# Kernel optimization log

Hardware: AMD Instinct MI355X
Metric: run time of the kernel (lower is better)

Reference implementation:

```python
import jax, jax.numpy as jnp
import numpy as np

N_NODES = 50000


def setup_inputs() -> dict:
    key = jax.random.key(0)
    k1, k2, k3, k4, k5, k6 = jax.random.split(key, 6)
    N, E, D, F = 50000, 800000, 512, 256
    feature_ori = jax.random.normal(k1, (N, D), dtype=jnp.float32)
    feature_aug = jax.random.normal(k2, (N, D), dtype=jnp.float32)
    edge_row = jax.random.randint(k3, (E,), 0, N, dtype=jnp.int32)
    edge_col = jax.random.randint(k4, (E,), 0, N, dtype=jnp.int32)
    edge_val = jax.random.uniform(k5, (E,), dtype=jnp.float32)
    # kaiming-uniform-ish init for weight, zeros for bias (as in reset_parameters)
    bound = float(np.sqrt(6.0 / D))
    weight = jax.random.uniform(k6, (D, F), dtype=jnp.float32, minval=-bound, maxval=bound)
    bias = jnp.zeros((F,), dtype=jnp.float32)
    return {
        "feature_ori": feature_ori,
        "feature_aug": feature_aug,
        "edge_row": edge_row,
        "edge_col": edge_col,
        "edge_val": edge_val,
        "weight": weight,
        "bias": bias,
    }


def _branch(feat, weight, bias, edge_row, edge_col, edge_val):
    # support = X @ W  -> [N, F]
    support = feat @ weight
    # sparse aggregation: out[i] = sum_{e: row[e]=i} val[e] * support[col[e]]
    msgs = edge_val[:, None] * support[edge_col]          # [E, F]
    out = jax.ops.segment_sum(msgs, edge_row, num_segments=N_NODES)
    return jax.nn.relu(out + bias)


def reference(feature_ori, feature_aug, edge_row, edge_col, edge_val, weight, bias):
    out_ori = _branch(feature_ori, weight, bias, edge_row, edge_col, edge_val)
    out_aug = _branch(feature_aug, weight, bias, edge_row, edge_col, edge_val)
    return (out_ori, out_aug)
```

## Files before the change

kernel.cpp:

```cpp
#include <hip/hip_runtime.h>
#include <hip/hip_bf16.h>

#define NNODES 50000
#define NEDGES 800000
#define DIN    512
#define FOUT   256

typedef __attribute__((ext_vector_type(8))) short short8;
typedef __attribute__((ext_vector_type(4))) float f32x4;
typedef __attribute__((ext_vector_type(4))) unsigned int u32x4;
typedef __attribute__((ext_vector_type(4))) unsigned short usv4;
typedef __attribute__((ext_vector_type(8))) unsigned short usv8;

static __device__ __forceinline__ unsigned short f2bf(float f) {
    unsigned int u = __float_as_uint(f);
    u += 0x7FFF + ((u >> 16) & 1);
    return (unsigned short)(u >> 16);
}
static __device__ __forceinline__ float bf2f(unsigned short h) {
    return __uint_as_float(((unsigned int)h) << 16);
}

__global__ void prep_kernel(const float* __restrict__ W, unsigned short* __restrict__ Wt,
                            const int* __restrict__ row, int* __restrict__ cnt) {
    int b = blockIdx.x;
    if (b < 512) {
        int o = b * 256 + threadIdx.x;
        int n = o >> 9, k = o & 511;
        Wt[o] = f2bf(W[k * FOUT + n]);
    } else {
        int e = (b - 512) * 256 + threadIdx.x;
        if (e < NEDGES) atomicAdd(&cnt[row[e]], 1);
    }
}

__global__ void scan_partial(const int* __restrict__ cnt, int* __restrict__ partial) {
    __shared__ int sm[256];
    int i = blockIdx.x * 256 + threadIdx.x;
    int v = (i < NNODES) ? cnt[i] : 0;
    sm[threadIdx.x] = v; __syncthreads();
    for (int s = 128; s > 0; s >>= 1) {
        if (threadIdx.x < s) sm[threadIdx.x] += sm[threadIdx.x + s];
        __syncthreads();
    }
    if (threadIdx.x == 0) partial[blockIdx.x] = sm[0];
}

__global__ void scan_exclusive_small(int* __restrict__ partial, int nb) {
    __shared__ int sm[256];
    int t = threadIdx.x;
    int v = (t < nb) ? partial[t] : 0;
    sm[t] = v; __syncthreads();
    for (int off = 1; off < 256; off <<= 1) {
        int add = (t >= off) ? sm[t - off] : 0;
        __syncthreads();
        sm[t] += add;
        __syncthreads();
    }
    if (t < nb) partial[t] = sm[t] - v;
}

__global__ void scan_write(const int* __restrict__ cnt, const int* __restrict__ partial,
                           int* __restrict__ row_start, int* __restrict__ cursor) {
    __shared__ int sm[256];
    int t = threadIdx.x;
    int i = blockIdx.x * 256 + t;
    int v = (i < NNODES) ? cnt[i] : 0;
    sm[t] = v; __syncthreads();
    for (int off = 1; off < 256; off <<= 1) {
        int add = (t >= off) ? sm[t - off] : 0;
        __syncthreads();
        sm[t] += add;
        __syncthreads();
    }
    if (i < NNODES) {
        int rs = partial[blockIdx.x] + sm[t] - v;
        row_start[i] = rs;
        cursor[i] = rs;
    }
    if (i == 0) row_start[NNODES] = NEDGES;
}

__global__ void scatter_kernel(const int* __restrict__ row, const int* __restrict__ col,
                               const float* __restrict__ val,
                               int* __restrict__ cursor, unsigned int* __restrict__ cv) {
    int e = blockIdx.x * 256 + threadIdx.x;
    if (e < NEDGES) {
        int r = row[e];
        int pos = atomicAdd(&cursor[r], 1);
        unsigned int vb = f2bf(val[e]);
        cv[pos] = (vb << 16) | (unsigned int)col[e];
    }
}

__global__ __launch_bounds__(256, 3)
void gemm_kernel(const float* __restrict__ Xo, const float* __restrict__ Xa,
                 const unsigned short* __restrict__ Wt,
                 unsigned short* __restrict__ S) {
    __shared__ __align__(16) unsigned short As[2][64][40];
    __shared__ __align__(16) unsigned short Bs[2][256][40];
    const int tid = threadIdx.x;
    const int branch = blockIdx.z;
    const float* __restrict__ X = branch ? Xa : Xo;
    const int boff = branch * 256;
    const int m_base = blockIdx.x * 64;
    const int lane = tid & 63, wave = tid >> 6;
    const int wn = wave * 64;
    const int quad = lane >> 4, r16 = lane & 15;

    f32x4 acc[4][4] = {};

    const int arow = tid >> 2;
    const int acol = (tid & 3) * 8;

    const int gm = m_base + arow;
    const bool va = gm < NNODES;
    const float* pA = &X[(long)gm * DIN + acol];
    const unsigned short* pB0 = &Wt[(long)(arow) * DIN + acol];
    const unsigned short* pB1 = &Wt[(long)(64 + arow) * DIN + acol];
    const unsigned short* pB2 = &Wt[(long)(128 + arow) * DIN + acol];
    const unsigned short* pB3 = &Wt[(long)(192 + arow) * DIN + acol];

    f32x4 fa0, fa1;
    u32x4 ub0, ub1, ub2, ub3;

#define GEMM_LOAD(K0)                                                          \
    do {                                                                       \
        fa0 = va ? __builtin_nontemporal_load((const f32x4*)(pA + (K0)))       \
                 : (f32x4)0.f;                                                 \
        fa1 = va ? __builtin_nontemporal_load((const f32x4*)(pA + (K0) + 4))   \
                 : (f32x4)0.f;                                                 \
        ub0 = *(const u32x4*)(pB0 + (K0));                                     \
        ub1 = *(const u32x4*)(pB1 + (K0));                                     \
        ub2 = *(const u32x4*)(pB2 + (K0));                                     \
        ub3 = *(const u32x4*)(pB3 + (K0));                                     \
    } while (0)

#define GEMM_WRITE(B)                                                          \
    do {                                                                       \
        usv8 h;                                                                \
        h[0] = f2bf(fa0[0]); h[1] = f2bf(fa0[1]);                              \
        h[2] = f2bf(fa0[2]); h[3] = f2bf(fa0[3]);                              \
        h[4] = f2bf(fa1[0]); h[5] = f2bf(fa1[1]);                              \
        h[6] = f2bf(fa1[2]); h[7] = f2bf(fa1[3]);                              \
        *(usv8*)&As[B][arow][acol] = h;                                        \
        *(u32x4*)&Bs[B][arow][acol] = ub0;                                     \
        *(u32x4*)&Bs[B][64 + arow][acol] = ub1;                                \
        *(u32x4*)&Bs[B][128 + arow][acol] = ub2;                               \
        *(u32x4*)&Bs[B][192 + arow][acol] = ub3;                               \
    } while (0)

#define GEMM_COMPUTE(B)                                                        \
    do {                                                                       \
        short8 a_frag[4], b_frag[4];                                           \
        _Pragma("unroll")                                                      \
        for (int mi = 0; mi < 4; mi++)                                         \
            a_frag[mi] = *(const short8*)&As[B][mi * 16 + r16][quad * 8];      \
        _Pragma("unroll")                                                      \
        for (int ni = 0; ni < 4; ni++)                                         \
            b_frag[ni] = *(const short8*)&Bs[B][wn + ni * 16 + r16][quad * 8]; \
        _Pragma("unroll")                                                      \
        for (int mi = 0; mi < 4; mi++)                                         \
            _Pragma("unroll")                                                  \
            for (int ni = 0; ni < 4; ni++)                                     \
                acc[mi][ni] = __builtin_amdgcn_mfma_f32_16x16x32_bf16(         \
                    a_frag[mi], b_frag[ni], acc[mi][ni], 0, 0, 0);             \
    } while (0)

#define GEMM_BARRIER()                                                         \
    do {                                                                       \
        asm volatile("s_waitcnt lgkmcnt(0)" ::: "memory");                     \
        __builtin_amdgcn_s_barrier();                                          \
        __builtin_amdgcn_sched_barrier(0);                                     \
    } while (0)

    GEMM_LOAD(0);
    GEMM_WRITE(0);
    GEMM_LOAD(32);
    GEMM_BARRIER();

    #pragma unroll
    for (int t = 0; t < 16; ++t) {
        if (t < 15) GEMM_WRITE((t + 1) & 1);
        if (t + 2 < 16) GEMM_LOAD((t + 2) * 32);
        GEMM_COMPUTE(t & 1);
        if (t < 15) GEMM_BARRIER();
    }

#undef GEMM_LOAD
#undef GEMM_WRITE
#undef GEMM_COMPUTE
#undef GEMM_BARRIER

    #pragma unroll
    for (int mi = 0; mi < 4; mi++) {
        #pragma unroll
        for (int rr = 0; rr < 4; rr++) {
            int m = m_base + mi * 16 + quad * 4 + rr;
            if (m < NNODES) {
                #pragma unroll
                for (int ni = 0; ni < 4; ni++) {
                    int n = wn + ni * 16 + r16;
                    S[(long)m * 512 + boff + n] = f2bf(acc[mi][ni][rr]);
                }
            }
        }
    }
}

__global__ __launch_bounds__(256)
void aggregate_pass(const int* __restrict__ row_start,
                    const unsigned int* __restrict__ cv,
                    const unsigned short* __restrict__ S,
                    const float* __restrict__ bias, float* __restrict__ out,
                    const int half) {
    const int node = __builtin_amdgcn_readfirstlane(blockIdx.x * 4 + (threadIdx.x >> 6));
    if (node >= NNODES) return;
    const int lane = threadIdx.x & 63;
    const int fl = (lane & 31) * 8;
    const unsigned int sub = lane >> 5;
    const long soff = (long)half * 256 + fl;
    const int s = row_start[node], e = row_start[node + 1];

    float a0 = 0.f, a1 = 0.f, a2 = 0.f, a3 = 0.f;
    float a4 = 0.f, a5 = 0.f, a6 = 0.f, a7 = 0.f;

#define PLOAD(CW0, CW1, Q)                                                     \
    do {                                                                       \
        unsigned int cw_ = sub ? (CW1) : (CW0);                                \
        Q = *(const usv8*)&S[(long)(cw_ & 0xFFFFu) * 512 + soff];              \
    } while (0)

#define PFMA(CW0, CW1, Q)                                                      \
    do {                                                                       \
        unsigned int cw_ = sub ? (CW1) : (CW0);                                \
        float v = bf2f((unsigned short)(cw_ >> 16));                           \
        a0 = fmaf(v, bf2f((Q)[0]), a0); a1 = fmaf(v, bf2f((Q)[1]), a1);        \
        a2 = fmaf(v, bf2f((Q)[2]), a2); a3 = fmaf(v, bf2f((Q)[3]), a3);        \
        a4 = fmaf(v, bf2f((Q)[4]), a4); a5 = fmaf(v, bf2f((Q)[5]), a5);        \
        a6 = fmaf(v, bf2f((Q)[6]), a6); a7 = fmaf(v, bf2f((Q)[7]), a7);        \
    } while (0)

#define LOADG(C0, C1, C2, C3, C4, C5, C6, C7, Q0, Q1, Q2, Q3, I)               \
    do {                                                                       \
        C0 = cv[(I)];     C1 = cv[(I) + 1]; C2 = cv[(I) + 2]; C3 = cv[(I) + 3];\
        C4 = cv[(I) + 4]; C5 = cv[(I) + 5]; C6 = cv[(I) + 6]; C7 = cv[(I) + 7];\
        PLOAD(C0, C1, Q0); PLOAD(C2, C3, Q1);                                  \
        PLOAD(C4, C5, Q2); PLOAD(C6, C7, Q3);                                  \
    } while (0)

#define FMAG(C0, C1, C2, C3, C4, C5, C6, C7, Q0, Q1, Q2, Q3)                   \
    do {                                                                       \
        PFMA(C0, C1, Q0); PFMA(C2, C3, Q1);                                    \
        PFMA(C4, C5, Q2); PFMA(C6, C7, Q3);                                    \
    } while (0)

    unsigned int c0, c1, c2, c3, c4, c5, c6, c7;
    unsigned int d0, d1, d2, d3, d4, d5, d6, d7;
    usv8 qa0, qa1, qa2, qa3, qb0, qb1, qb2, qb3;

    int idx = s;
    int r = (e - s) >> 3;
    if (r > 0) {
        LOADG(c0, c1, c2, c3, c4, c5, c6, c7, qa0, qa1, qa2, qa3, idx); idx += 8; r--;
        while (r >= 2) {
            LOADG(d0, d1, d2, d3, d4, d5, d6, d7, qb0, qb1, qb2, qb3, idx); idx += 8;
            FMAG(c0, c1, c2, c3, c4, c5, c6, c7, qa0, qa1, qa2, qa3);
            LOADG(c0, c1, c2, c3, c4, c5, c6, c7, qa0, qa1, qa2, qa3, idx); idx += 8;
            FMAG(d0, d1, d2, d3, d4, d5, d6, d7, qb0, qb1, qb2, qb3);
            r -= 2;
        }
        if (r == 1) {
            LOADG(d0, d1, d2, d3, d4, d5, d6, d7, qb0, qb1, qb2, qb3, idx); idx += 8;
            FMAG(c0, c1, c2, c3, c4, c5, c6, c7, qa0, qa1, qa2, qa3);
            FMAG(d0, d1, d2, d3, d4, d5, d6, d7, qb0, qb1, qb2, qb3);
        } else {
            FMAG(c0, c1, c2, c3, c4, c5, c6, c7, qa0, qa1, qa2, qa3);
        }
    }
    for (; idx + 2 <= e; idx += 2) {
        unsigned int w0 = cv[idx], w1 = cv[idx + 1];
        usv8 q;
        PLOAD(w0, w1, q);
        PFMA(w0, w1, q);
    }
    if (idx < e) {
        unsigned int w = cv[idx];
        usv8 q = *(const usv8*)&S[(long)(w & 0xFFFFu) * 512 + soff];
        float v = sub ? 0.f : bf2f((unsigned short)(w >> 16));
        a0 = fmaf(v, bf2f(q[0]), a0); a1 = fmaf(v, bf2f(q[1]), a1);
        a2 = fmaf(v, bf2f(q[2]), a2); a3 = fmaf(v, bf2f(q[3]), a3);
        a4 = fmaf(v, bf2f(q[4]), a4); a5 = fmaf(v, bf2f(q[5]), a5);
        a6 = fmaf(v, bf2f(q[6]), a6); a7 = fmaf(v, bf2f(q[7]), a7);
    }

#undef PLOAD
#undef PFMA
#undef LOADG
#undef FMAG

    a0 += __shfl_xor(a0, 32); a1 += __shfl_xor(a1, 32);
    a2 += __shfl_xor(a2, 32); a3 += __shfl_xor(a3, 32);
    a4 += __shfl_xor(a4, 32); a5 += __shfl_xor(a5, 32);
    a6 += __shfl_xor(a6, 32); a7 += __shfl_xor(a7, 32);

    if (lane < 32) {
        f32x4 b0 = *(const f32x4*)&bias[fl];
        f32x4 b1 = *(const f32x4*)&bias[fl + 4];
        long o = (long)half * NNODES * FOUT + (long)node * FOUT + fl;
        f32x4 r0, r1;
        r0[0] = fmaxf(a0 + b0[0], 0.f); r0[1] = fmaxf(a1 + b0[1], 0.f);
        r0[2] = fmaxf(a2 + b0[2], 0.f); r0[3] = fmaxf(a3 + b0[3], 0.f);
        r1[0] = fmaxf(a4 + b1[0], 0.f); r1[1] = fmaxf(a5 + b1[1], 0.f);
        r1[2] = fmaxf(a6 + b1[2], 0.f); r1[3] = fmaxf(a7 + b1[3], 0.f);
        __builtin_nontemporal_store(r0, (f32x4*)&out[o]);
        __builtin_nontemporal_store(r1, (f32x4*)&out[o + 4]);
    }
}

extern "C" void kernel_launch(void* const* d_in, const int* in_sizes, int n_in,
                              void* d_out, int out_size, void* d_ws, size_t ws_size,
                              hipStream_t stream) {
    const float* Xo   = (const float*)d_in[0];
    const float* Xa   = (const float*)d_in[1];
    const int*   erow = (const int*)d_in[2];
    const int*   ecol = (const int*)d_in[3];
    const float* eval_= (const float*)d_in[4];
    const float* W    = (const float*)d_in[5];
    const float* bias = (const float*)d_in[6];
    float* out = (float*)d_out;

    char* ws = (char*)d_ws;
    unsigned short* S         = (unsigned short*)(ws);
    unsigned short* Wt        = (unsigned short*)(ws + 51200000);
    int*            cnt       = (int*)(ws + 51462144);
    int*            row_start = (int*)(ws + 51662144);
    int*            partial   = (int*)(ws + 51862208);
    unsigned int*   cv        = (unsigned int*)(ws + 51863232);

    (void)in_sizes; (void)n_in; (void)out_size; (void)ws_size;

    hipMemsetAsync(cnt, 0, 200000, stream);
    prep_kernel<<<3637, 256, 0, stream>>>(W, Wt, erow, cnt);
    scan_partial<<<196, 256, 0, stream>>>(cnt, partial);
    scan_exclusive_small<<<1, 256, 0, stream>>>(partial, 196);
    scan_write<<<196, 256, 0, stream>>>(cnt, partial, row_start, cnt);
    scatter_kernel<<<3125, 256, 0, stream>>>(erow, ecol, eval_, cnt, cv);

    dim3 gg(782, 1, 2);
    gemm_kernel<<<gg, 256, 0, stream>>>(Xo, Xa, Wt, S);

    aggregate_pass<<<12500, 256, 0, stream>>>(row_start, cv, S, bias, out, 0);
    aggregate_pass<<<12500, 256, 0, stream>>>(row_start, cv, S, bias, out, 1);
}
```

Measured before the change: 484.8 us.

## Enlarge GEMM block tile to 128x256 with 2x2 wave layout

The GEMM block tile grows from 64 rows to 128 rows. Waves are rearranged into a 2x2 grid, each computing 64x128 with 32 accumulators. This halves the number of blocks and the redundant W-tile loads per output row, and raises MFMA work per LDS fragment load. In exchange it uses more registers and LDS per block, lowers occupancy (launch bounds 3 to 2), and leaves fewer blocks for tail balancing.

```diff
diff --git a/kernel.cpp b/kernel.cpp
--- a/kernel.cpp
+++ b/kernel.cpp
@@ -93,35 +93,31 @@
     }
 }
 
-__global__ __launch_bounds__(256, 3)
+__global__ __launch_bounds__(256, 2)
 void gemm_kernel(const float* __restrict__ Xo, const float* __restrict__ Xa,
                  const unsigned short* __restrict__ Wt,
                  unsigned short* __restrict__ S) {
-    __shared__ __align__(16) unsigned short As[2][64][40];
+    __shared__ __align__(16) unsigned short As[2][128][40];
     __shared__ __align__(16) unsigned short Bs[2][256][40];
     const int tid = threadIdx.x;
     const int branch = blockIdx.z;
     const float* __restrict__ X = branch ? Xa : Xo;
     const int boff = branch * 256;
-    const int m_base = blockIdx.x * 64;
+    const int m_base = blockIdx.x * 128;
     const int lane = tid & 63, wave = tid >> 6;
-    const int wn = wave * 64;
+    const int wm = (wave >> 1) * 64, wn = (wave & 1) * 128;
     const int quad = lane >> 4, r16 = lane & 15;
 
-    f32x4 acc[4][4] = {};
-
-    const int arow = tid >> 2;
-    const int acol = (tid & 3) * 8;
-
+    f32x4 acc[4][8] = {};
+
+    const int arow = tid >> 1;
+    const int acol = (tid & 1) * 16;
     const int gm = m_base + arow;
     const bool va = gm < NNODES;
     const float* pA = &X[(long)gm * DIN + acol];
-    const unsigned short* pB0 = &Wt[(long)(arow) * DIN + acol];
-    const unsigned short* pB1 = &Wt[(long)(64 + arow) * DIN + acol];
-    const unsigned short* pB2 = &Wt[(long)(128 + arow) * DIN + acol];
-    const unsigned short* pB3 = &Wt[(long)(192 + arow) * DIN + acol];
-
-    f32x4 fa0, fa1;
+    const unsigned short* pB = &Wt[(long)tid * DIN];
+
+    f32x4 fa0, fa1, fa2, fa3;
     u32x4 ub0, ub1, ub2, ub3;
 
 #define GEMM_LOAD(K0)                                                          \
@@ -130,41 +126,51 @@
                  : (f32x4)0.f;                                                 \
         fa1 = va ? __builtin_nontemporal_load((const f32x4*)(pA + (K0) + 4))   \
                  : (f32x4)0.f;                                                 \
-        ub0 = *(const u32x4*)(pB0 + (K0));                                     \
-        ub1 = *(const u32x4*)(pB1 + (K0));                                     \
-        ub2 = *(const u32x4*)(pB2 + (K0));                                     \
-        ub3 = *(const u32x4*)(pB3 + (K0));                                     \
+        fa2 = va ? __builtin_nontemporal_load((const f32x4*)(pA + (K0) + 8))   \
+                 : (f32x4)0.f;                                                 \
+        fa3 = va ? __builtin_nontemporal_load((const f32x4*)(pA + (K0) + 12))  \
+                 : (f32x4)0.f;                                                 \
+        ub0 = *(const u32x4*)(pB + (K0));                                      \
+        ub1 = *(const u32x4*)(pB + (K0) + 8);                                  \
+        ub2 = *(const u32x4*)(pB + (K0) + 16);                                 \
+        ub3 = *(const u32x4*)(pB + (K0) + 24);                                 \
     } while (0)
 
 #define GEMM_WRITE(B)                                                          \
     do {                                                                       \
-        usv8 h;                                                                \
-        h[0] = f2bf(fa0[0]); h[1] = f2bf(fa0[1]);                              \
-        h[2] = f2bf(fa0[2]); h[3] = f2bf(fa0[3]);                              \
-        h[4] = f2bf(fa1[0]); h[5] = f2bf(fa1[1]);                              \
-        h[6] = f2bf(fa1[2]); h[7] = f2bf(fa1[3]);                              \
-        *(usv8*)&As[B][arow][acol] = h;                                        \
-        *(u32x4*)&Bs[B][arow][acol] = ub0;                                     \
-        *(u32x4*)&Bs[B][64 + arow][acol] = ub1;                                \
-        *(u32x4*)&Bs[B][128 + arow][acol] = ub2;                               \
-        *(u32x4*)&Bs[B][192 + arow][acol] = ub3;                               \
+        usv8 h0;                                                               \
+        h0[0] = f2bf(fa0[0]); h0[1] = f2bf(fa0[1]);                            \
+        h0[2] = f2bf(fa0[2]); h0[3] = f2bf(fa0[3]);                            \
+        h0[4] = f2bf(fa1[0]); h0[5] = f2bf(fa1[1]);                            \
+        h0[6] = f2bf(fa1[2]); h0[7] = f2bf(fa1[3]);                            \
+        *(usv8*)&As[B][arow][acol] = h0;                                       \
+        usv8 h1;                                                               \
+        h1[0] = f2bf(fa2[0]); h1[1] = f2bf(fa2[1]);                            \
+        h1[2] = f2bf(fa2[2]); h1[3] = f2bf(fa2[3]);                            \
+        h1[4] = f2bf(fa3[0]); h1[5] = f2bf(fa3[1]);                            \
+        h1[6] = f2bf(fa3[2]); h1[7] = f2bf(fa3[3]);                            \
+        *(usv8*)&As[B][arow][acol + 8] = h1;                                   \
+        *(u32x4*)&Bs[B][tid][0]  = ub0;                                        \
+        *(u32x4*)&Bs[B][tid][8]  = ub1;                                        \
+        *(u32x4*)&Bs[B][tid][16] = ub2;                                        \
+        *(u32x4*)&Bs[B][tid][24] = ub3;                                        \
     } while (0)
 
 #define GEMM_COMPUTE(B)                                                        \
     do {                                                                       \
-        short8 a_frag[4], b_frag[4];                                           \
+        short8 a_frag[4];                                                      \
         _Pragma("unroll")                                                      \
         for (int mi = 0; mi < 4; mi++)                                         \
-            a_frag[mi] = *(const short8*)&As[B][mi * 16 + r16][quad * 8];      \
+            a_frag[mi] = *(const short8*)&As[B][wm + mi * 16 + r16][quad * 8]; \
         _Pragma("unroll")                                                      \
-        for (int ni = 0; ni < 4; ni++)                                         \
-            b_frag[ni] = *(const short8*)&Bs[B][wn + ni * 16 + r16][quad * 8]; \
-        _Pragma("unroll")                                                      \
-        for (int mi = 0; mi < 4; mi++)                                         \
+        for (int ni = 0; ni < 8; ni++) {                                       \
+            short8 b_frag =                                                    \
+                *(const short8*)&Bs[B][wn + ni * 16 + r16][quad * 8];          \
             _Pragma("unroll")                                                  \
-            for (int ni = 0; ni < 4; ni++)                                     \
+            for (int mi = 0; mi < 4; mi++)                                     \
                 acc[mi][ni] = __builtin_amdgcn_mfma_f32_16x16x32_bf16(         \
-                    a_frag[mi], b_frag[ni], acc[mi][ni], 0, 0, 0);             \
+                    a_frag[mi], b_frag, acc[mi][ni], 0, 0, 0);                 \
+        }                                                                      \
     } while (0)
 
 #define GEMM_BARRIER()                                                         \
@@ -196,10 +202,10 @@
     for (int mi = 0; mi < 4; mi++) {
         #pragma unroll
         for (int rr = 0; rr < 4; rr++) {
-            int m = m_base + mi * 16 + quad * 4 + rr;
+            int m = m_base + wm + mi * 16 + quad * 4 + rr;
             if (m < NNODES) {
                 #pragma unroll
-                for (int ni = 0; ni < 4; ni++) {
+                for (int ni = 0; ni < 8; ni++) {
                     int n = wn + ni * 16 + r16;
                     S[(long)m * 512 + boff + n] = f2bf(acc[mi][ni][rr]);
                 }
@@ -347,7 +353,7 @@
     scan_write<<<196, 256, 0, stream>>>(cnt, partial, row_start, cnt);
     scatter_kernel<<<3125, 256, 0, stream>>>(erow, ecol, eval_, cnt, cv);
 
-    dim3 gg(782, 1, 2);
+    dim3 gg(391, 1, 2);
     gemm_kernel<<<gg, 256, 0, stream>>>(Xo, Xa, Wt, S);
 
     aggregate_pass<<<12500, 256, 0, stream>>>(row_start, cv, S, bias, out, 0);
```

New measurement: 516.2 us. 6.5% more time.
